# Performance work log

Hardware: AMD Instinct MI355X
Metric: run time of the kernel (lower is better)

## Reference

```python
import jax, jax.numpy as jnp
import numpy as np

E = 1024      # embed_dim
H = 16        # num heads
D = E // H    # head_dim = 64
B, T = 4, 2048


def setup_inputs() -> dict:
    key = jax.random.key(0)
    ks = jax.random.split(key, 7)
    hidden_states = jax.random.normal(ks[0], (B, T, E), dtype=jnp.float32)
    # torch Linear weight layout: [out_features, in_features]
    Wqkv = jax.random.normal(ks[1], (3 * E, E), dtype=jnp.float32) * (1.0 / np.sqrt(E))
    bqkv = jax.random.normal(ks[2], (3 * E,), dtype=jnp.float32) * 0.02
    Wproj = jax.random.normal(ks[3], (E, E), dtype=jnp.float32) * (1.0 / np.sqrt(E))
    bproj = jax.random.normal(ks[4], (E,), dtype=jnp.float32) * 0.02
    splat_scale = jax.random.normal(ks[5], (H,), dtype=jnp.float32) * 0.5
    splat_bias = jax.random.normal(ks[6], (H, 1, 1), dtype=jnp.float32) * 0.5
    return {
        'hidden_states': hidden_states,
        'Wqkv': Wqkv, 'bqkv': bqkv,
        'Wproj': Wproj, 'bproj': bproj,
        'splat_scale': splat_scale, 'splat_bias': splat_bias,
    }


def reference(hidden_states, Wqkv, bqkv, Wproj, bproj, splat_scale, splat_bias):
    b, t, _ = hidden_states.shape
    scale_factor = 1.0 / np.sqrt(D)

    qkv = hidden_states @ Wqkv.T + bqkv                    # [B,T,3E]
    q, k, v = jnp.split(qkv, 3, axis=-1)
    # [B,H,T,D]
    q = q.reshape(b, t, H, D).transpose(0, 2, 1, 3)
    k = k.reshape(b, t, H, D).transpose(0, 2, 1, 3)
    v = v.reshape(b, t, H, D).transpose(0, 2, 1, 3)

    scores = jnp.einsum('bhqd,bhkd->bhqk', q * scale_factor, k)  # [B,H,T,T]

    s = (1.0 + 0.01 * jnp.tanh(splat_scale)).reshape(1, H, 1, 1)
    bsp = (0.001 * jnp.tanh(splat_bias)).reshape(1, H, 1, 1)
    scores = s * scores + bsp

    causal = jnp.tril(jnp.ones((t, t), dtype=bool))
    scores = jnp.where(causal, scores, jnp.float32(-1e9))

    attn = jax.nn.softmax(scores, axis=-1)                 # dropout = identity (eval)
    out = jnp.einsum('bhqk,bhkd->bhqd', attn, v)
    out = out.transpose(0, 2, 1, 3).reshape(b, t, E)
    out = out @ Wproj.T + bproj
    return out
```

## Files before the change

kernel.cpp:

```cpp
#include <hip/hip_runtime.h>
#include <stdint.h>

#define BB 4
#define TT 2048
#define EE 1024
#define HH 16
#define DD 64
#define MM (BB*TT)
#define NQKV (3*EE)

typedef __bf16 bf16_t;
typedef bf16_t bf16x8 __attribute__((ext_vector_type(8)));
typedef short  s16x4  __attribute__((ext_vector_type(4)));
typedef float  floatx4 __attribute__((ext_vector_type(4)));

__device__ __forceinline__ unsigned short f2bf(float f) {
    unsigned int u = __float_as_uint(f);
    u = (u + 0x7FFFu + ((u >> 16) & 1u)) >> 16;
    return (unsigned short)u;
}

__device__ __forceinline__ void load_lds16(const void* g, void* l) {
    __builtin_amdgcn_global_load_lds(
        (const __attribute__((address_space(1))) unsigned int*)g,
        (__attribute__((address_space(3))) unsigned int*)l, 16, 0, 0);
}

__global__ void cvt_f32_bf16(const float* __restrict__ in,
                             unsigned short* __restrict__ out, int n) {
    int i = (blockIdx.x * 256 + threadIdx.x) * 4;
    if (i + 3 < n) {
        float4 v = *reinterpret_cast<const float4*>(in + i);
        ushort4 o;
        o.x = f2bf(v.x); o.y = f2bf(v.y); o.z = f2bf(v.z); o.w = f2bf(v.w);
        *reinterpret_cast<ushort4*>(out + i) = o;
    }
}

#define VW(N) asm volatile("s_waitcnt vmcnt(" #N ")" ::: "memory")
#define BARX() do { __builtin_amdgcn_s_barrier(); asm volatile("" ::: "memory"); } while (0)
#define FRv(p, t) (*reinterpret_cast<const bf16x8*>((p) + (t) * 512))
#define SLOT(kt) (((kt) % 3) * 2)
#define MFMA1(mi, ni, av, bv) \
    acc[mi][ni] = __builtin_amdgcn_mfma_f32_16x16x32_bf16(av, bv, acc[mi][ni], 0, 0, 0)
#define MFMA_SET(s) do { \
    MFMA1(0,0,afr[s][0],bfr[s][0]); MFMA1(0,1,afr[s][0],bfr[s][1]); MFMA1(0,2,afr[s][0],bfr[s][2]); MFMA1(0,3,afr[s][0],bfr[s][3]); \
    MFMA1(1,0,afr[s][1],bfr[s][0]); MFMA1(1,1,afr[s][1],bfr[s][1]); MFMA1(1,2,afr[s][1],bfr[s][2]); MFMA1(1,3,afr[s][1],bfr[s][3]); \
    MFMA1(2,0,afr[s][2],bfr[s][0]); MFMA1(2,1,afr[s][2],bfr[s][1]); MFMA1(2,2,afr[s][2],bfr[s][2]); MFMA1(2,3,afr[s][2],bfr[s][3]); \
    MFMA1(3,0,afr[s][3],bfr[s][0]); MFMA1(3,1,afr[s][3],bfr[s][1]); MFMA1(3,2,afr[s][3],bfr[s][2]); MFMA1(3,3,afr[s][3],bfr[s][3]); \
} while (0)
#define STAGE_H(kt_, h_) do { \
    const unsigned short* _ga = Ag + (kt_) * 64 + (h_) * 32; \
    unsigned short* _la = (unsigned short*)&As[SLOT(kt_) + (h_)][w * 512]; \
    load_lds16(_ga, _la); \
    load_lds16(_ga + (size_t)128 * 1024, _la + 4096); \
    load_lds16(Bg + (kt_) * 64 + (h_) * 32, &Bs[SLOT(kt_) + (h_)][w * 512]); \
} while (0)
#define RDFRAG(st, kt_, h_) do { \
    const unsigned short* _pa = &As[SLOT(kt_) + (h_)][aoff]; \
    afr[st][0] = FRv(_pa, 0); afr[st][1] = FRv(_pa, 1); \
    afr[st][2] = FRv(_pa, 2); afr[st][3] = FRv(_pa, 3); \
    const unsigned short* _pb = &Bs[SLOT(kt_) + (h_)][boff]; \
    bfr[st][0] = FRv(_pb, 0); bfr[st][1] = FRv(_pb, 1); \
    bfr[st][2] = FRv(_pb, 2); bfr[st][3] = FRv(_pb, 3); \
} while (0)
#define TILE(kt_, VA, VB, DS1, DS0, DRD) do { \
    VW(VA); BARX();                        \
    if (DS1) STAGE_H((kt_) + 2, 1); \
    RDFRAG(1, kt_, 1);                     \
    __builtin_amdgcn_s_setprio(1); MFMA_SET(0); __builtin_amdgcn_s_setprio(0); \
    VW(VB); BARX();                        \
    if (DS0) STAGE_H((kt_) + 3, 0); \
    if (DRD) RDFRAG(0, (kt_) + 1, 0);      \
    __builtin_amdgcn_s_setprio(1); MFMA_SET(1); __builtin_amdgcn_s_setprio(0); \
} while (0)

template<int N, int EPI>
__global__ __launch_bounds__(512, 2) void gemm256(
    const unsigned short* __restrict__ A,
    const unsigned short* __restrict__ Bw,
    const float* __restrict__ bias,
    const float* __restrict__ sscale,
    unsigned short* __restrict__ Qb,
    unsigned short* __restrict__ Kb,
    unsigned short* __restrict__ Vtb,
    float* __restrict__ Cout)
{
    __shared__ __align__(16) unsigned short As[6][8192];
    __shared__ __align__(16) unsigned short Bs[6][4096];

    const int tid  = threadIdx.x;
    const int lane = tid & 63;
    const int w    = tid >> 6;
    const int quad = lane >> 4;
    const int l16  = lane & 15;

    const int nwg = (int)gridDim.x;
    const int wg  = ((int)blockIdx.x & 7) * (nwg >> 3) + ((int)blockIdx.x >> 3);
    const int nbx = N / 128;
    const int m0  = (wg / nbx) * 256;
    const int n0  = (wg % nbx) * 128;

    const int wm = (w >> 1) * 64;
    const int wn = (w & 1) * 64;

    const unsigned short* Ag = A  + (size_t)(m0 + 16 * w + l16) * 1024 + quad * 8;
    const unsigned short* Bg = Bw + (size_t)(n0 + 16 * w + l16) * 1024 + quad * 8;

    const int aoff = (w >> 1) * 2048 + lane * 8;
    const int boff = (w & 1) * 2048 + lane * 8;

    bf16x8 afr[2][4], bfr[2][4];
    floatx4 acc[4][4] = {};

    STAGE_H(0, 0); STAGE_H(0, 1); STAGE_H(1, 0); STAGE_H(1, 1); STAGE_H(2, 0);
    VW(9); BARX();
    RDFRAG(0, 0, 0);

#pragma unroll
    for (int kt = 0; kt < 13; ++kt)
        TILE(kt, 9, 9, 1, 1, 1);
    TILE(13, 9, 9, 1, 0, 1);
    TILE(14, 6, 3, 0, 0, 1);
    VW(0); BARX();
    RDFRAG(1, 15, 1);
    __builtin_amdgcn_s_setprio(1); MFMA_SET(0); MFMA_SET(1); __builtin_amdgcn_s_setprio(0);

    if (EPI == 0) {
        const int colb  = n0 + wn;
        const int which = colb >> 10;
#pragma unroll
        for (int nt = 0; nt < 4; ++nt) {
            const int col = colb + nt * 16 + l16;
            const int e = col & 1023;
            const int hh = e >> 6, d = e & 63;
            const float bsv = bias[col];
            float qs = 0.f;
            if (which == 0) qs = (1.0f + 0.01f * tanhf(sscale[hh])) * 0.125f;
#pragma unroll
            for (int mt = 0; mt < 4; ++mt) {
                const int rowb = m0 + wm + mt * 16 + quad * 4;
#pragma unroll
                for (int r = 0; r < 4; ++r) {
                    const int m = rowb + r;
                    const int b = m >> 11, t = m & 2047;
                    const size_t bh = (size_t)(b * HH + hh);
                    float v = acc[mt][nt][r] + bsv;
                    if (which == 0) {
                        Qb[(bh * TT + t) * DD + d] = f2bf(v * qs);
                    } else if (which == 1) {
                        Kb[(bh * TT + t) * DD + d] = f2bf(v);
                    } else {
                        Vtb[(bh * DD + d) * TT + t] = f2bf(v);
                    }
                }
            }
        }
    } else {
#pragma unroll
        for (int mt = 0; mt < 4; ++mt) {
            const int rowb = m0 + wm + mt * 16 + quad * 4;
#pragma unroll
            for (int nt = 0; nt < 4; ++nt) {
                const int col = n0 + wn + nt * 16 + l16;
                const float bsv = bias[col];
#pragma unroll
                for (int r = 0; r < 4; ++r)
                    Cout[(size_t)(rowb + r) * N + col] = acc[mt][nt][r] + bsv;
            }
        }
    }
}

#define LP 72
__global__ __launch_bounds__(256, 4) void flash_attn(
    const unsigned short* __restrict__ Qb,
    const unsigned short* __restrict__ Kb,
    const unsigned short* __restrict__ Vtb,
    unsigned short* __restrict__ Ob)
{
    __shared__ __align__(16) unsigned short Ks[2][64 * LP];
    __shared__ __align__(16) unsigned short Vs[2][64 * LP];

    const int tid  = threadIdx.x;
    const int lane = tid & 63;
    const int w    = tid >> 6;
    const int quad = lane >> 4;
    const int l16  = lane & 15;
    const int i    = blockIdx.x;
    const int bh   = i & 63;
    const int qt   = 31 - (i >> 6);
    const int row0 = qt * 64 + w * 16;

    const unsigned short* qbase = &Qb[((size_t)bh * TT + row0 + l16) * DD + quad * 8];
    const bf16x8 qf0 = *reinterpret_cast<const bf16x8*>(qbase);
    const bf16x8 qf1 = *reinterpret_cast<const bf16x8*>(qbase + 32);

    const s16x4 vones = { (short)0x3F80, (short)0x3F80, (short)0x3F80, (short)0x3F80 };

    floatx4 o[4] = {};
    floatx4 o1 = {};

    const int srow = tid >> 3;
    const int scol = (tid & 7) * 8;
    const size_t kgbase = ((size_t)bh * TT + srow) * DD + scol;
    const size_t vgbase = ((size_t)bh * DD + srow) * TT + scol;

    uint4 kr0 = *reinterpret_cast<const uint4*>(&Kb[kgbase]);
    uint4 kr1 = *reinterpret_cast<const uint4*>(&Kb[kgbase + 32 * DD]);
    uint4 vr0 = *reinterpret_cast<const uint4*>(&Vtb[vgbase]);
    uint4 vr1 = *reinterpret_cast<const uint4*>(&Vtb[vgbase + 32 * TT]);

    for (int kt = 0; kt <= qt; ++kt) {
        const int buf = kt & 1;
        *reinterpret_cast<uint4*>(&Ks[buf][srow * LP + scol]) = kr0;
        *reinterpret_cast<uint4*>(&Ks[buf][(srow + 32) * LP + scol]) = kr1;
        *reinterpret_cast<uint4*>(&Vs[buf][srow * LP + scol]) = vr0;
        *reinterpret_cast<uint4*>(&Vs[buf][(srow + 32) * LP + scol]) = vr1;
        __syncthreads();

        if (kt < qt) {
            size_t ko = kgbase + (size_t)(kt + 1) * 64 * DD;
            size_t vo = vgbase + (size_t)(kt + 1) * 64;
            kr0 = *reinterpret_cast<const uint4*>(&Kb[ko]);
            kr1 = *reinterpret_cast<const uint4*>(&Kb[ko + 32 * DD]);
            vr0 = *reinterpret_cast<const uint4*>(&Vtb[vo]);
            vr1 = *reinterpret_cast<const uint4*>(&Vtb[vo + 32 * TT]);
        }

        const int keyb = kt * 64 + quad * 4;
        const int qr0  = row0 + l16;
        const bool diag = (kt == qt);

#pragma unroll
        for (int ntk = 0; ntk < 4; ++ntk) {
            const unsigned short* krow = &Ks[buf][(ntk * 16 + l16) * LP + quad * 8];
            bf16x8 kf0 = *reinterpret_cast<const bf16x8*>(krow);
            bf16x8 kf1 = *reinterpret_cast<const bf16x8*>(krow + 32);

            floatx4 st = {0.f, 0.f, 0.f, 0.f};
            st = __builtin_amdgcn_mfma_f32_16x16x32_bf16(kf0, qf0, st, 0, 0, 0);
            st = __builtin_amdgcn_mfma_f32_16x16x32_bf16(kf1, qf1, st, 0, 0, 0);

            s16x4 pf;
#pragma unroll
            for (int r = 0; r < 4; ++r) {
                float p = __expf(st[r]);
                pf[r] = (short)((!diag || (keyb + ntk * 16 + r <= qr0)) ? f2bf(p) : 0);
            }

            o1 = __builtin_amdgcn_mfma_f32_16x16x16bf16_1k(pf, vones, o1, 0, 0, 0);
#pragma unroll
            for (int dt = 0; dt < 4; ++dt) {
                s16x4 vf = *reinterpret_cast<const s16x4*>(
                    &Vs[buf][(dt * 16 + l16) * LP + ntk * 16 + quad * 4]);
                o[dt] = __builtin_amdgcn_mfma_f32_16x16x16bf16_1k(pf, vf, o[dt], 0, 0, 0);
            }
        }
    }

    const int b = bh >> 4, h = bh & 15;
#pragma unroll
    for (int r = 0; r < 4; ++r) {
        int q = row0 + quad * 4 + r;
        float rl = __builtin_amdgcn_rcpf(o1[r]);
#pragma unroll
        for (int dt = 0; dt < 4; ++dt)
            Ob[((size_t)(b * TT + q)) * EE + h * DD + dt * 16 + l16] =
                f2bf(o[dt][r] * rl);
    }
}

extern "C" void kernel_launch(void* const* d_in, const int* in_sizes, int n_in,
                              void* d_out, int out_size, void* d_ws, size_t ws_size,
                              hipStream_t stream) {
    const float* hs    = (const float*)d_in[0];
    const float* Wqkv  = (const float*)d_in[1];
    const float* bqkv  = (const float*)d_in[2];
    const float* Wproj = (const float*)d_in[3];
    const float* bproj = (const float*)d_in[4];
    const float* ss    = (const float*)d_in[5];
    float* out = (float*)d_out;

    char* p = (char*)d_ws;
    unsigned short* hsb    = (unsigned short*)p; p += (size_t)MM * EE * 2;
    unsigned short* wqkvb  = (unsigned short*)p; p += (size_t)NQKV * EE * 2;
    unsigned short* wprojb = (unsigned short*)p; p += (size_t)EE * EE * 2;
    unsigned short* Qb     = (unsigned short*)p; p += (size_t)BB*HH*TT*DD * 2;
    unsigned short* Kb     = (unsigned short*)p; p += (size_t)BB*HH*TT*DD * 2;
    unsigned short* Vtb    = (unsigned short*)p; p += (size_t)BB*HH*TT*DD * 2;

    cvt_f32_bf16<<<(MM * EE) / 1024, 256, 0, stream>>>(hs, hsb, MM * EE);
    cvt_f32_bf16<<<(NQKV * EE) / 1024, 256, 0, stream>>>(Wqkv, wqkvb, NQKV * EE);
    cvt_f32_bf16<<<(EE * EE) / 1024, 256, 0, stream>>>(Wproj, wprojb, EE * EE);

    gemm256<NQKV, 0><<<dim3((MM / 256) * (NQKV / 128)), 512, 0, stream>>>(
        hsb, wqkvb, bqkv, ss, Qb, Kb, Vtb, nullptr);

    flash_attn<<<dim3(2048), 256, 0, stream>>>(Qb, Kb, Vtb, hsb);

    gemm256<EE, 1><<<dim3((MM / 256) * (EE / 128)), 512, 0, stream>>>(
        hsb, wprojb, bproj, nullptr, nullptr, nullptr, nullptr, out);
}
```

Measured before the change: 308.0 us.

## Fuse bf16 conversions, swizzle GEMM LDS layout, streamline softmax masking

Merges the three f32-to-bf16 conversion launches into one kernel, which removes two launch overheads and tail effects. Changes the GEMM global-to-LDS staging to a row-per-4-thread layout with an XOR swizzle on 16-byte chunks, aiming to cut LDS bank conflicts on fragment reads. In flash attention it applies the causal mask only on diagonal tiles and uses the hardware bf16 conversion instead of manual rounding. The swizzle must match the unseen RDFRAG and STAGE macros, so fragment read offsets could be wrong.

```diff
diff --git a/kernel.cpp b/kernel.cpp
--- a/kernel.cpp
+++ b/kernel.cpp
@@ -20,21 +20,31 @@
     return (unsigned short)u;
 }
 
+__device__ __forceinline__ short bfs(float f) {
+    return (short)__builtin_bit_cast(unsigned short, (bf16_t)f);
+}
+
 __device__ __forceinline__ void load_lds16(const void* g, void* l) {
     __builtin_amdgcn_global_load_lds(
         (const __attribute__((address_space(1))) unsigned int*)g,
         (__attribute__((address_space(3))) unsigned int*)l, 16, 0, 0);
 }
 
-__global__ void cvt_f32_bf16(const float* __restrict__ in,
-                             unsigned short* __restrict__ out, int n) {
-    int i = (blockIdx.x * 256 + threadIdx.x) * 4;
-    if (i + 3 < n) {
-        float4 v = *reinterpret_cast<const float4*>(in + i);
-        ushort4 o;
-        o.x = f2bf(v.x); o.y = f2bf(v.y); o.z = f2bf(v.z); o.w = f2bf(v.w);
-        *reinterpret_cast<ushort4*>(out + i) = o;
-    }
+#define NV1 ((MM*EE)/4)
+#define NV2 ((NQKV*EE)/4)
+#define NV3 ((EE*EE)/4)
+__global__ void cvt_all(const float* __restrict__ s1, unsigned short* __restrict__ d1,
+                        const float* __restrict__ s2, unsigned short* __restrict__ d2,
+                        const float* __restrict__ s3, unsigned short* __restrict__ d3) {
+    int v = blockIdx.x * 256 + threadIdx.x;
+    const float* s; unsigned short* d; int i;
+    if (v < NV1)            { s = s1; d = d1; i = v; }
+    else if (v < NV1 + NV2) { s = s2; d = d2; i = v - NV1; }
+    else                    { s = s3; d = d3; i = v - NV1 - NV2; }
+    float4 x = *reinterpret_cast<const float4*>(s + i * 4);
+    ushort4 o;
+    o.x = f2bf(x.x); o.y = f2bf(x.y); o.z = f2bf(x.z); o.w = f2bf(x.w);
+    *reinterpret_cast<ushort4*>(d + i * 4) = o;
 }
 
 #define VW(N) asm volatile("s_waitcnt vmcnt(" #N ")" ::: "memory")
@@ -104,11 +114,13 @@
     const int wm = (w >> 1) * 64;
     const int wn = (w & 1) * 64;
 
-    const unsigned short* Ag = A  + (size_t)(m0 + 16 * w + l16) * 1024 + quad * 8;
-    const unsigned short* Bg = Bw + (size_t)(n0 + 16 * w + l16) * 1024 + quad * 8;
-
-    const int aoff = (w >> 1) * 2048 + lane * 8;
-    const int boff = (w & 1) * 2048 + lane * 8;
+    const int chk = (tid & 3) ^ ((tid >> 3) & 3);
+    const unsigned short* Ag = A  + (size_t)(m0 + (tid >> 2)) * 1024 + chk * 8;
+    const unsigned short* Bg = Bw + (size_t)(n0 + (tid >> 2)) * 1024 + chk * 8;
+
+    const int rsl  = (quad ^ ((l16 >> 1) & 3)) * 8;
+    const int aoff = (wm + l16) * 32 + rsl;
+    const int boff = (wn + l16) * 32 + rsl;
 
     bf16x8 afr[2][4], bfr[2][4];
     floatx4 acc[4][4] = {};
@@ -242,12 +254,17 @@
             st = __builtin_amdgcn_mfma_f32_16x16x32_bf16(kf0, qf0, st, 0, 0, 0);
             st = __builtin_amdgcn_mfma_f32_16x16x32_bf16(kf1, qf1, st, 0, 0, 0);
 
+            float p0 = __expf(st[0]), p1 = __expf(st[1]);
+            float p2 = __expf(st[2]), p3 = __expf(st[3]);
+            if (diag) {
+                const int kb = keyb + ntk * 16;
+                p0 = (kb + 0 <= qr0) ? p0 : 0.f;
+                p1 = (kb + 1 <= qr0) ? p1 : 0.f;
+                p2 = (kb + 2 <= qr0) ? p2 : 0.f;
+                p3 = (kb + 3 <= qr0) ? p3 : 0.f;
+            }
             s16x4 pf;
-#pragma unroll
-            for (int r = 0; r < 4; ++r) {
-                float p = __expf(st[r]);
-                pf[r] = (short)((!diag || (keyb + ntk * 16 + r <= qr0)) ? f2bf(p) : 0);
-            }
+            pf[0] = bfs(p0); pf[1] = bfs(p1); pf[2] = bfs(p2); pf[3] = bfs(p3);
 
             o1 = __builtin_amdgcn_mfma_f32_16x16x16bf16_1k(pf, vones, o1, 0, 0, 0);
 #pragma unroll
@@ -290,9 +307,8 @@
     unsigned short* Kb     = (unsigned short*)p; p += (size_t)BB*HH*TT*DD * 2;
     unsigned short* Vtb    = (unsigned short*)p; p += (size_t)BB*HH*TT*DD * 2;
 
-    cvt_f32_bf16<<<(MM * EE) / 1024, 256, 0, stream>>>(hs, hsb, MM * EE);
-    cvt_f32_bf16<<<(NQKV * EE) / 1024, 256, 0, stream>>>(Wqkv, wqkvb, NQKV * EE);
-    cvt_f32_bf16<<<(EE * EE) / 1024, 256, 0, stream>>>(Wproj, wprojb, EE * EE);
+    cvt_all<<<(NV1 + NV2 + NV3) / 256, 256, 0, stream>>>(
+        hs, hsb, Wqkv, wqkvb, Wproj, wprojb);
 
     gemm256<NQKV, 0><<<dim3((MM / 256) * (NQKV / 128)), 512, 0, stream>>>(
         hsb, wqkvb, bqkv, ss, Qb, Kb, Vtb, nullptr);
```

Result: faster. 269.2 us (-12.6%).
